# Performance work log

Measured on AMD Instinct MI355X. Metric: run time of the kernel, lower is better.

The kernel has to match this reference:

```python
import jax, jax.numpy as jnp
import numpy as np

N, L, H, E, D = 8, 1024, 16, 1024, 64  # batch, seq_len, heads, embed_size, head_dim


def _xavier(k, shape):
    fan_out, fan_in = shape
    lim = np.sqrt(6.0 / (fan_in + fan_out)).astype(np.float32)
    return jax.random.uniform(k, shape, jnp.float32, -lim, lim)


def setup_inputs() -> dict:
    key = jax.random.key(0)
    ks = jax.random.split(key, 6)
    return {
        "x": jax.random.normal(ks[0], (N, L, E, 1), jnp.float32),
        "Wq": _xavier(ks[1], (D, D)), "bq": jnp.zeros((D,), jnp.float32),
        "Wk": _xavier(ks[2], (D, D)), "bk": jnp.zeros((D,), jnp.float32),
        "Wv": _xavier(ks[3], (D, D)), "bv": jnp.zeros((D,), jnp.float32),
        "Erel": jax.random.normal(ks[4], (1, L, D), jnp.float32),
        "Wo": _xavier(ks[5], (E, E)), "bo": jnp.zeros((E,), jnp.float32),
    }


def _skew(qe):
    # qe: [N, H, L, L] -> pad one zero col on the left, reshape, drop first row
    n, h, l, _ = qe.shape
    p = jnp.pad(qe, ((0, 0), (0, 0), (0, 0), (1, 0)))  # [N,H,L,L+1]
    p = p.reshape(n, h, l + 1, l)
    return p[:, :, 1:, :]  # [N,H,L,L]


def reference(x, Wq, bq, Wk, bk, Wv, bv, Erel, Wo, bo):
    x0 = x[:, :, :, 0]                      # [N, L, E]
    z = x0.reshape(N, L, H, D)              # [N, L, H, D]
    q = z @ Wq.T + bq
    k = z @ Wk.T + bk
    v = z @ Wv.T + bv
    # QE = queries.transpose(1,2) @ E.transpose(1,2): [N,H,L,D] @ [D,L] -> [N,H,L,L]
    QE = jnp.einsum('nlhd,td->nhlt', q, Erel[0])
    # mask_positions: zero where triu(ones,1).flip(1) == 1
    mask = jnp.flip(jnp.triu(jnp.ones((L, L), jnp.float32), 1), axis=1)
    QE = jnp.where(mask == 1, 0.0, QE)
    S = _skew(QE)                           # [N,H,L,L]
    qk = jnp.einsum('nqhd,nkhd->nhqk', q, k)
    attention = jax.nn.softmax(qk / jnp.sqrt(jnp.float32(E)), axis=3) + S
    out = jnp.einsum('nhql,nlhd->nqhd', attention, v).reshape(N, L, H * D)
    return out @ Wo.T + bo                  # [N, L, E]
```

## Files before the change

kernel.cpp:

```cpp
#include <hip/hip_runtime.h>
#include <math.h>

#define N_ 8
#define L_ 1024
#define H_ 16
#define E_ 1024
#define D_ 64

typedef __bf16 bf16x8 __attribute__((ext_vector_type(8)));
typedef __bf16 bf16x4 __attribute__((ext_vector_type(4)));
typedef float  f32x4  __attribute__((ext_vector_type(4)));

#define MFMA16(a, b, c) __builtin_amdgcn_mfma_f32_16x16x32_bf16((a), (b), (c), 0, 0, 0)

#define KSCALE 0.04508422002778011f

__global__ __launch_bounds__(256) void prep_kernel(
    const float* __restrict__ Wo, const float* __restrict__ Erel,
    __bf16* __restrict__ wobf, __bf16* __restrict__ erbf)
{
    const int idx = blockIdx.x * 256 + threadIdx.x;
    const float* src;
    __bf16* dst;
    int off;
    if (blockIdx.x < 1024) { src = Wo;   dst = wobf; off = idx * 4; }
    else                   { src = Erel; dst = erbf; off = (idx - 1024 * 256) * 4; }
    const float4 f = *(const float4*)(src + off);
    bf16x4 h;
    h[0] = (__bf16)f.x; h[1] = (__bf16)f.y; h[2] = (__bf16)f.z; h[3] = (__bf16)f.w;
    *(bf16x4*)(dst + off) = h;
}

__global__ __launch_bounds__(256) void qkv_kernel(
    const float* __restrict__ x,
    const float* __restrict__ Wq, const float* __restrict__ bq,
    const float* __restrict__ Wk, const float* __restrict__ bk,
    const float* __restrict__ Wv, const float* __restrict__ bv,
    __bf16* __restrict__ qo, __bf16* __restrict__ ko, __bf16* __restrict__ vo)
{
    const int t = threadIdx.x, w = t >> 6, lane = t & 63;
    const int quad = lane >> 4, l16 = lane & 15;
    const int m0 = blockIdx.x * 64;

    __shared__ __bf16 xs[64][72];
    __shared__ __bf16 wls[3][64][72];

    #pragma unroll
    for (int i = 0; i < 4; ++i) {
        const int idx = t + i * 256, row = idx >> 4, c4 = idx & 15;
        {
            const float4 f = *(const float4*)(x + (size_t)(m0 + row) * 64 + c4 * 4);
            bf16x4 hh; hh[0]=(__bf16)f.x; hh[1]=(__bf16)f.y; hh[2]=(__bf16)f.z; hh[3]=(__bf16)f.w;
            *(bf16x4*)&xs[row][c4 * 4] = hh;
        }
        {
            const float4 f = *(const float4*)(Wq + (size_t)row * 64 + c4 * 4);
            bf16x4 hh; hh[0]=(__bf16)f.x; hh[1]=(__bf16)f.y; hh[2]=(__bf16)f.z; hh[3]=(__bf16)f.w;
            *(bf16x4*)&wls[0][row][c4 * 4] = hh;
        }
        {
            const float4 f = *(const float4*)(Wk + (size_t)row * 64 + c4 * 4);
            bf16x4 hh; hh[0]=(__bf16)f.x; hh[1]=(__bf16)f.y; hh[2]=(__bf16)f.z; hh[3]=(__bf16)f.w;
            *(bf16x4*)&wls[1][row][c4 * 4] = hh;
        }
        {
            const float4 f = *(const float4*)(Wv + (size_t)row * 64 + c4 * 4);
            bf16x4 hh; hh[0]=(__bf16)f.x; hh[1]=(__bf16)f.y; hh[2]=(__bf16)f.z; hh[3]=(__bf16)f.w;
            *(bf16x4*)&wls[2][row][c4 * 4] = hh;
        }
    }
    __syncthreads();

    bf16x8 a[2];
    a[0] = *(const bf16x8*)&xs[w * 16 + l16][quad * 8];
    a[1] = *(const bf16x8*)&xs[w * 16 + l16][32 + quad * 8];

    f32x4 acc[12];
    const f32x4 zero4 = {0.f, 0.f, 0.f, 0.f};
    #pragma unroll
    for (int nt = 0; nt < 12; ++nt) acc[nt] = zero4;

    #pragma unroll
    for (int nt = 0; nt < 12; ++nt) {
        const int sel = nt >> 2, dt = nt & 3;
        #pragma unroll
        for (int c = 0; c < 2; ++c) {
            const bf16x8 b = *(const bf16x8*)&wls[sel][dt * 16 + l16][c * 32 + quad * 8];
            acc[nt] = MFMA16(a[c], b, acc[nt]);
        }
    }
    __syncthreads();

    __bf16* ts = &wls[0][0][0];
    const float* bias[3] = {bq, bk, bv};
    __bf16* outp[3] = {qo, ko, vo};
    #pragma unroll
    for (int nt = 0; nt < 12; ++nt) {
        const int sel = nt >> 2, dt = nt & 3;
        const float bb = bias[sel][dt * 16 + l16];
        const float scl = (sel == 1) ? KSCALE : 1.0f;
        #pragma unroll
        for (int r = 0; r < 4; ++r)
            ts[(size_t)(w * 16 + quad * 4 + r) * 208 + sel * 64 + dt * 16 + l16] =
                (__bf16)((acc[nt][r] + bb) * scl);
    }
    __syncthreads();
    #pragma unroll
    for (int sel = 0; sel < 3; ++sel)
        #pragma unroll
        for (int i = 0; i < 2; ++i) {
            const int idx = t * 2 + i, row = idx >> 3, c = idx & 7;
            *(float4*)(outp[sel] + (size_t)(m0 + row) * 64 + c * 8) =
                *(const float4*)&ts[(size_t)row * 208 + sel * 64 + c * 8];
        }
}

__global__ __launch_bounds__(256) void vtr_kernel(
    const __bf16* __restrict__ v, __bf16* __restrict__ vt)
{
    const int bid = blockIdx.x;
    const int lt = bid & 15, h = (bid >> 4) & 15, n = bid >> 8;
    const int l0 = lt * 64;
    const int t = threadIdx.x;
    __shared__ __bf16 ls[64][72];

    const int lrow = t & 63, c0 = t >> 6;
    #pragma unroll
    for (int i = 0; i < 2; ++i) {
        const int c = c0 + i * 4;
        union { float4 f; __bf16 hv[8]; } u;
        u.f = *(const float4*)(v + ((size_t)(n * L_ + l0 + lrow) * H_ + h) * D_ + c * 8);
        #pragma unroll
        for (int j = 0; j < 8; ++j) ls[c * 8 + j][lrow] = u.hv[j];
    }
    __syncthreads();
    const int drow0 = t >> 3, lc = t & 7;
    #pragma unroll
    for (int i = 0; i < 2; ++i) {
        const int d = drow0 + i * 32;
        *(float4*)(vt + ((size_t)(n * H_ + h) * D_ + d) * L_ + l0 + lc * 8) =
            *(const float4*)&ls[d][lc * 8];
    }
}

__global__ __launch_bounds__(512, 4) void rel_kernel(
    const __bf16* __restrict__ qbf, const __bf16* __restrict__ vtrb,
    const __bf16* __restrict__ erbf, __bf16* __restrict__ rbuf)
{
    const int bid = blockIdx.x;
    const int qt = 3 - (bid >> 7);
    const int p = bid & 127;
    const int h = p & 15, n = p >> 4;
    const int q0 = qt * 256;
    const int t = threadIdx.x, w = t >> 6, lane = t & 63;
    const int quad = lane >> 4, l16 = lane & 15;

    __shared__ __bf16 vt[2][64][72];
    __shared__ __bf16 rs[128][72];

    const int qA = q0 + w * 16;
    const size_t qoffA = ((size_t)(n * L_ + qA + l16) * H_ + h) * D_;
    const size_t qoffB = qoffA + (size_t)128 * H_ * D_;
    const bf16x8 qaA0 = *(const bf16x8*)(qbf + qoffA + quad * 8);
    const bf16x8 qaA1 = *(const bf16x8*)(qbf + qoffA + 32 + quad * 8);
    const bf16x8 qaB0 = *(const bf16x8*)(qbf + qoffB + quad * 8);
    const bf16x8 qaB1 = *(const bf16x8*)(qbf + qoffB + 32 + quad * 8);

    const __bf16* vbase = vtrb + ((size_t)(n * H_ + h) * D_) * L_;
    const int srow = t >> 3, sc8 = (t & 7) * 8;
    const int ktmax = qt * 4 + 4;

    float4 vreg = *(const float4*)(vbase + (size_t)srow * 1024 + sc8);
    *(float4*)&vt[0][srow][sc8] = vreg;
    vreg = *(const float4*)(vbase + 64 + (size_t)srow * 1024 + sc8);
    __syncthreads();

    const f32x4 zero4 = {0.f, 0.f, 0.f, 0.f};
    f32x4 OrA[4], OrB[4];
    #pragma unroll
    for (int nt = 0; nt < 4; ++nt) { OrA[nt] = zero4; OrB[nt] = zero4; }

    for (int kt = 0; kt < ktmax; ++kt) {
        const int cur = kt & 1;
        if (kt + 1 < ktmax) {
            *(float4*)&vt[cur ^ 1][srow][sc8] = vreg;
            if (kt + 2 < ktmax)
                vreg = *(const float4*)(vbase + (kt + 2) * 64
                                        + (size_t)srow * 1024 + sc8);
        }

        const bool dorelA = (kt * 64 <= qA + 15);
        const bool dorelB = (kt * 64 <= qA + 128 + 15);
        bf16x8 rbA0, rbA1, rbB0, rbB1;

        if (dorelA) {
            const int tb = kt * 64 + 1008 - qA;
            #pragma unroll
            for (int st = 0; st < 5; ++st) {
                int tr = tb + st * 16 + l16;
                tr = tr > 1023 ? 1023 : tr;
                const __bf16* er = erbf + (size_t)tr * 64;
                f32x4 acc = zero4;
                acc = MFMA16(*(const bf16x8*)(er + quad * 8), qaA0, acc);
                acc = MFMA16(*(const bf16x8*)(er + 32 + quad * 8), qaA1, acc);
                #pragma unroll
                for (int r = 0; r < 4; ++r) {
                    const int kc = st * 16 + quad * 4 + r + l16 - 15;
                    const int tg = tb + st * 16 + quad * 4 + r;
                    if (kc >= 0 && kc < 64)
                        rs[w * 16 + l16][kc] = (tg <= 1023) ? (__bf16)acc[r]
                                                            : (__bf16)0.0f;
                }
            }
            rbA0 = *(const bf16x8*)&rs[w * 16 + l16][quad * 8];
            rbA1 = *(const bf16x8*)&rs[w * 16 + l16][32 + quad * 8];
        }
        if (dorelB) {
            const int tb = kt * 64 + 1008 - (qA + 128);
            #pragma unroll
            for (int st = 0; st < 5; ++st) {
                int tr = tb + st * 16 + l16;
                tr = tr > 1023 ? 1023 : tr;
                const __bf16* er = erbf + (size_t)tr * 64;
                f32x4 acc = zero4;
                acc = MFMA16(*(const bf16x8*)(er + quad * 8), qaB0, acc);
                acc = MFMA16(*(const bf16x8*)(er + 32 + quad * 8), qaB1, acc);
                #pragma unroll
                for (int r = 0; r < 4; ++r) {
                    const int kc = st * 16 + quad * 4 + r + l16 - 15;
                    const int tg = tb + st * 16 + quad * 4 + r;
                    if (kc >= 0 && kc < 64)
                        rs[w * 16 + l16][kc] = (tg <= 1023) ? (__bf16)acc[r]
                                                            : (__bf16)0.0f;
                }
            }
            rbB0 = *(const bf16x8*)&rs[w * 16 + l16][quad * 8];
            rbB1 = *(const bf16x8*)&rs[w * 16 + l16][32 + quad * 8];
        }

        #pragma unroll
        for (int nt = 0; nt < 4; ++nt) {
            const bf16x8 va0 = *(const bf16x8*)&vt[cur][nt * 16 + l16][quad * 8];
            const bf16x8 va1 = *(const bf16x8*)&vt[cur][nt * 16 + l16][32 + quad * 8];
            if (dorelA) {
                OrA[nt] = MFMA16(va0, rbA0, OrA[nt]);
                OrA[nt] = MFMA16(va1, rbA1, OrA[nt]);
            }
            if (dorelB) {
                OrB[nt] = MFMA16(va0, rbB0, OrB[nt]);
                OrB[nt] = MFMA16(va1, rbB1, OrB[nt]);
            }
        }
        __syncthreads();
    }

    const int erow = lane >> 3, ec8 = lane & 7;
    #pragma unroll
    for (int nt = 0; nt < 4; ++nt) {
        bf16x4 ov;
        #pragma unroll
        for (int r = 0; r < 4; ++r) ov[r] = (__bf16)OrA[nt][r];
        *(bf16x4*)&rs[w * 16 + l16][nt * 16 + quad * 4] = ov;
    }
    #pragma unroll
    for (int i = 0; i < 2; ++i) {
        const int r = erow + i * 8;
        *(float4*)(rbuf + ((size_t)(n * L_ + qA + r)) * E_ + h * 64 + ec8 * 8) =
            *(const float4*)&rs[w * 16 + r][ec8 * 8];
    }
    #pragma unroll
    for (int nt = 0; nt < 4; ++nt) {
        bf16x4 ov;
        #pragma unroll
        for (int r = 0; r < 4; ++r) ov[r] = (__bf16)OrB[nt][r];
        *(bf16x4*)&rs[w * 16 + l16][nt * 16 + quad * 4] = ov;
    }
    #pragma unroll
    for (int i = 0; i < 2; ++i) {
        const int r = erow + i * 8;
        *(float4*)(rbuf + ((size_t)(n * L_ + qA + 128 + r)) * E_ + h * 64 + ec8 * 8) =
            *(const float4*)&rs[w * 16 + r][ec8 * 8];
    }
}

__global__ __launch_bounds__(512, 4) void flash_kernel(
    const __bf16* __restrict__ qbf, const __bf16* __restrict__ kbf,
    const __bf16* __restrict__ vtrb, const __bf16* __restrict__ rbuf,
    __bf16* __restrict__ attnA)
{
    const int bid = blockIdx.x;
    const int qt = bid >> 7;
    const int p = bid & 127;
    const int h = p & 15, n = p >> 4;
    const int q0 = qt * 256;
    const int t = threadIdx.x, w = t >> 6, lane = t & 63;
    const int quad = lane >> 4, l16 = lane & 15;

    __shared__ __bf16 ks[2][64][72];
    __shared__ __bf16 vt[2][64][72];
    __shared__ __bf16 ps[128][72];

    const int qA = q0 + w * 16;
    const size_t qoffA = ((size_t)(n * L_ + qA + l16) * H_ + h) * D_;
    const size_t qoffB = qoffA + (size_t)128 * H_ * D_;
    const bf16x8 qaA0 = *(const bf16x8*)(qbf + qoffA + quad * 8);
    const bf16x8 qaA1 = *(const bf16x8*)(qbf + qoffA + 32 + quad * 8);
    const bf16x8 qaB0 = *(const bf16x8*)(qbf + qoffB + quad * 8);
    const bf16x8 qaB1 = *(const bf16x8*)(qbf + qoffB + 32 + quad * 8);

    const __bf16* kbase = kbf + ((size_t)n * L_ * H_ + h) * D_;
    const __bf16* vbase = vtrb + ((size_t)(n * H_ + h) * D_) * L_;
    const int srow = t >> 3, sc8 = (t & 7) * 8;

    float4 kreg = *(const float4*)(kbase + (size_t)srow * 1024 + sc8);
    float4 vreg = *(const float4*)(vbase + (size_t)srow * 1024 + sc8);
    *(float4*)&ks[0][srow][sc8] = kreg;
    *(float4*)&vt[0][srow][sc8] = vreg;
    kreg = *(const float4*)(kbase + 64 * 1024 + (size_t)srow * 1024 + sc8);
    vreg = *(const float4*)(vbase + 64 + (size_t)srow * 1024 + sc8);
    __syncthreads();

    const f32x4 zero4 = {0.f, 0.f, 0.f, 0.f};
    f32x4 OsA[4], OsB[4];
    #pragma unroll
    for (int nt = 0; nt < 4; ++nt) { OsA[nt] = zero4; OsB[nt] = zero4; }
    float esumA = 0.f, esumB = 0.f;

    for (int kt = 0; kt < 16; ++kt) {
        const int cur = kt & 1;
        if (kt < 15) {
            *(float4*)&ks[cur ^ 1][srow][sc8] = kreg;
            *(float4*)&vt[cur ^ 1][srow][sc8] = vreg;
            if (kt < 14) {
                kreg = *(const float4*)(kbase + (size_t)(kt + 2) * 64 * 1024
                                        + (size_t)srow * 1024 + sc8);
                vreg = *(const float4*)(vbase + (kt + 2) * 64
                                        + (size_t)srow * 1024 + sc8);
            }
        }

        f32x4 sA[4], sB[4];
        #pragma unroll
        for (int nt = 0; nt < 4; ++nt) {
            const bf16x8 ka0 = *(const bf16x8*)&ks[cur][nt * 16 + l16][quad * 8];
            const bf16x8 ka1 = *(const bf16x8*)&ks[cur][nt * 16 + l16][32 + quad * 8];
            f32x4 a = zero4;
            a = MFMA16(ka0, qaA0, a);
            a = MFMA16(ka1, qaA1, a);
            sA[nt] = a;
            f32x4 b = zero4;
            b = MFMA16(ka0, qaB0, b);
            b = MFMA16(ka1, qaB1, b);
            sB[nt] = b;
        }

        #pragma unroll
        for (int nt = 0; nt < 4; ++nt) {
            bf16x4 pk;
            #pragma unroll
            for (int r = 0; r < 4; ++r) {
                const float e = exp2f(sA[nt][r]);
                esumA += e;
                pk[r] = (__bf16)e;
            }
            *(bf16x4*)&ps[w * 16 + l16][nt * 16 + quad * 4] = pk;
        }
        const bf16x8 pbA0 = *(const bf16x8*)&ps[w * 16 + l16][quad * 8];
        const bf16x8 pbA1 = *(const bf16x8*)&ps[w * 16 + l16][32 + quad * 8];
        #pragma unroll
        for (int nt = 0; nt < 4; ++nt) {
            bf16x4 pk;
            #pragma unroll
            for (int r = 0; r < 4; ++r) {
                const float e = exp2f(sB[nt][r]);
                esumB += e;
                pk[r] = (__bf16)e;
            }
            *(bf16x4*)&ps[w * 16 + l16][nt * 16 + quad * 4] = pk;
        }
        const bf16x8 pbB0 = *(const bf16x8*)&ps[w * 16 + l16][quad * 8];
        const bf16x8 pbB1 = *(const bf16x8*)&ps[w * 16 + l16][32 + quad * 8];

        #pragma unroll
        for (int nt = 0; nt < 4; ++nt) {
            const bf16x8 va0 = *(const bf16x8*)&vt[cur][nt * 16 + l16][quad * 8];
            const bf16x8 va1 = *(const bf16x8*)&vt[cur][nt * 16 + l16][32 + quad * 8];
            OsA[nt] = MFMA16(va0, pbA0, OsA[nt]);
            OsA[nt] = MFMA16(va1, pbA1, OsA[nt]);
            OsB[nt] = MFMA16(va0, pbB0, OsB[nt]);
            OsB[nt] = MFMA16(va1, pbB1, OsB[nt]);
        }
        __syncthreads();
    }

    esumA += __shfl_xor(esumA, 16, 64);
    esumA += __shfl_xor(esumA, 32, 64);
    esumB += __shfl_xor(esumB, 16, 64);
    esumB += __shfl_xor(esumB, 32, 64);
    const float invlA = 1.0f / esumA;
    const float invlB = 1.0f / esumB;
    const int erow = lane >> 3, ec8 = lane & 7;

    #pragma unroll
    for (int nt = 0; nt < 4; ++nt) {
        bf16x4 ov;
        #pragma unroll
        for (int r = 0; r < 4; ++r) ov[r] = (__bf16)(OsA[nt][r] * invlA);
        *(bf16x4*)&ps[w * 16 + l16][nt * 16 + quad * 4] = ov;
    }
    #pragma unroll
    for (int i = 0; i < 2; ++i) {
        const int r = erow + i * 8;
        const size_t goff = ((size_t)(n * L_ + qA + r)) * E_ + h * 64 + ec8 * 8;
        union { float4 f; __bf16 hv[8]; } ua, ub, uo;
        ua.f = *(const float4*)&ps[w * 16 + r][ec8 * 8];
        ub.f = *(const float4*)(rbuf + goff);
        #pragma unroll
        for (int j = 0; j < 8; ++j)
            uo.hv[j] = (__bf16)((float)ua.hv[j] + (float)ub.hv[j]);
        *(float4*)(attnA + goff) = uo.f;
    }
    #pragma unroll
    for (int nt = 0; nt < 4; ++nt) {
        bf16x4 ov;
        #pragma unroll
        for (int r = 0; r < 4; ++r) ov[r] = (__bf16)(OsB[nt][r] * invlB);
        *(bf16x4*)&ps[w * 16 + l16][nt * 16 + quad * 4] = ov;
    }
    #pragma unroll
    for (int i = 0; i < 2; ++i) {
        const int r = erow + i * 8;
        const size_t goff = ((size_t)(n * L_ + qA + 128 + r)) * E_ + h * 64 + ec8 * 8;
        union { float4 f; __bf16 hv[8]; } ua, ub, uo;
        ua.f = *(const float4*)&ps[w * 16 + r][ec8 * 8];
        ub.f = *(const float4*)(rbuf + goff);
        #pragma unroll
        for (int j = 0; j < 8; ++j)
            uo.hv[j] = (__bf16)((float)ua.hv[j] + (float)ub.hv[j]);
        *(float4*)(attnA + goff) = uo.f;
    }
}

__global__ __launch_bounds__(256) void proj_kernel(
    const __bf16* __restrict__ A, const __bf16* __restrict__ W,
    const float* __restrict__ bo, float* __restrict__ out)
{
    const int bid = blockIdx.x;
    const int rt = bid >> 3, ct = bid & 7;
    const int r0 = rt * 128, c0 = ct * 128;
    const int t = threadIdx.x, w = t >> 6, lane = t & 63;
    const int quad = lane >> 4, l16 = lane & 15;
    const int wm = w >> 1, wn = w & 1;

    __shared__ __bf16 As[128 * 64];
    __shared__ __bf16 Bs[128 * 64];

    f32x4 acc[16];
    const f32x4 zero4 = {0.f, 0.f, 0.f, 0.f};
    #pragma unroll
    for (int i = 0; i < 16; ++i) acc[i] = zero4;

    const int lrow = lane >> 3, lcg = lane & 7;

    for (int kt = 0; kt < 16; ++kt) {
        const int e0 = kt * 64;
        __syncthreads();
        #pragma unroll
        for (int i = 0; i < 4; ++i) {
            const int chunk = w * 4 + i;
            const int row = chunk * 8 + lrow;
            const __bf16* ga = A + (size_t)(r0 + row) * E_ + e0 + lcg * 8;
            const __bf16* gb = W + (size_t)(c0 + row) * E_ + e0 + lcg * 8;
            __builtin_amdgcn_global_load_lds(
                (const __attribute__((address_space(1))) void*)ga,
                (__attribute__((address_space(3))) void*)&As[chunk * 512], 16, 0, 0);
            __builtin_amdgcn_global_load_lds(
                (const __attribute__((address_space(1))) void*)gb,
                (__attribute__((address_space(3))) void*)&Bs[chunk * 512], 16, 0, 0);
        }
        __syncthreads();
        #pragma unroll
        for (int c = 0; c < 2; ++c) {
            bf16x8 am[4], bn[4];
            #pragma unroll
            for (int i = 0; i < 4; ++i) {
                am[i] = *(const bf16x8*)&As[(wm * 64 + i * 16 + l16) * 64 + c * 32 + quad * 8];
                bn[i] = *(const bf16x8*)&Bs[(wn * 64 + i * 16 + l16) * 64 + c * 32 + quad * 8];
            }
            #pragma unroll
            for (int i = 0; i < 4; ++i)
                #pragma unroll
                for (int j = 0; j < 4; ++j)
                    acc[i * 4 + j] = MFMA16(am[i], bn[j], acc[i * 4 + j]);
        }
    }

    #pragma unroll
    for (int i = 0; i < 4; ++i)
        #pragma unroll
        for (int j = 0; j < 4; ++j) {
            const int col = c0 + wn * 64 + j * 16 + l16;
            const float bb = bo[col];
            #pragma unroll
            for (int r = 0; r < 4; ++r)
                out[(size_t)(r0 + wm * 64 + i * 16 + quad * 4 + r) * E_ + col] =
                    acc[i * 4 + j][r] + bb;
        }
}

extern "C" void kernel_launch(void* const* d_in, const int* in_sizes, int n_in,
                              void* d_out, int out_size, void* d_ws, size_t ws_size,
                              hipStream_t stream)
{
    const float* x    = (const float*)d_in[0];
    const float* Wq   = (const float*)d_in[1];
    const float* bq   = (const float*)d_in[2];
    const float* Wk   = (const float*)d_in[3];
    const float* bk   = (const float*)d_in[4];
    const float* Wv   = (const float*)d_in[5];
    const float* bv   = (const float*)d_in[6];
    const float* Erel = (const float*)d_in[7];
    const float* Wo   = (const float*)d_in[8];
    const float* bo   = (const float*)d_in[9];
    float* out = (float*)d_out;

    char* p = (char*)d_ws;
    __bf16* qbf   = (__bf16*)p; p += (size_t)N_ * L_ * H_ * D_ * 2;
    __bf16* kbf   = (__bf16*)p; p += (size_t)N_ * L_ * H_ * D_ * 2;
    __bf16* vbf   = (__bf16*)p; p += (size_t)N_ * L_ * H_ * D_ * 2;
    __bf16* vtrb  = (__bf16*)p; p += (size_t)N_ * L_ * H_ * D_ * 2;
    __bf16* attnA = (__bf16*)p; p += (size_t)N_ * L_ * E_ * 2;
    __bf16* rbuf  = (__bf16*)p; p += (size_t)N_ * L_ * E_ * 2;
    __bf16* wobf  = (__bf16*)p; p += (size_t)E_ * E_ * 2;
    __bf16* erbf  = (__bf16*)p; p += (size_t)L_ * D_ * 2;

    prep_kernel<<<1088, 256, 0, stream>>>(Wo, Erel, wobf, erbf);
    qkv_kernel<<<(N_ * L_ * H_) / 64, 256, 0, stream>>>(x, Wq, bq, Wk, bk, Wv, bv,
                                                        qbf, kbf, vbf);
    vtr_kernel<<<N_ * H_ * (L_ / 64), 256, 0, stream>>>(vbf, vtrb);
    rel_kernel<<<512, 512, 0, stream>>>(qbf, vtrb, erbf, rbuf);
    flash_kernel<<<512, 512, 0, stream>>>(qbf, kbf, vtrb, rbuf, attnA);
    proj_kernel<<<(N_ * L_ / 128) * (E_ / 128), 256, 0, stream>>>(attnA, wobf, bo, out);
}
```

Measured before the change: 300.4 us.

## Fuse relative-position kernel into flash attention kernel, drop rbuf round trip

Merges rel_kernel into flash_kernel so the skewed QE·V term is accumulated in registers alongside the softmax·V term within the same K/V tile loop. This removes the bf16 rbuf intermediate (write and re-read of N·L·E) and one kernel launch, and reuses the V tiles already in shared memory. Erel is padded with zero rows so the clamping and masking branches go away, and the skew scatter writes into a widened ps buffer at an offset. In exchange the fused kernel uses more registers and shared memory, which may reduce occupancy, and the block ordering changes relative to the old causal-work scheduling.

```diff
diff --git a/kernel.cpp b/kernel.cpp
--- a/kernel.cpp
+++ b/kernel.cpp
@@ -15,16 +15,25 @@
 
 #define KSCALE 0.04508422002778011f
 
+#define ER_ROWS 1104
+
 __global__ __launch_bounds__(256) void prep_kernel(
     const float* __restrict__ Wo, const float* __restrict__ Erel,
     __bf16* __restrict__ wobf, __bf16* __restrict__ erbf)
 {
-    const int idx = blockIdx.x * 256 + threadIdx.x;
+    const int b = blockIdx.x;
+    const int idx = b * 256 + threadIdx.x;
+    if (b >= 1088) {
+        const int off = (idx - 1088 * 256) * 4;
+        bf16x4 z; z[0] = z[1] = z[2] = z[3] = (__bf16)0.0f;
+        *(bf16x4*)(erbf + 1024 * 64 + off) = z;
+        return;
+    }
     const float* src;
     __bf16* dst;
     int off;
-    if (blockIdx.x < 1024) { src = Wo;   dst = wobf; off = idx * 4; }
-    else                   { src = Erel; dst = erbf; off = (idx - 1024 * 256) * 4; }
+    if (b < 1024) { src = Wo;   dst = wobf; off = idx * 4; }
+    else          { src = Erel; dst = erbf; off = (idx - 1024 * 256) * 4; }
     const float4 f = *(const float4*)(src + off);
     bf16x4 h;
     h[0] = (__bf16)f.x; h[1] = (__bf16)f.y; h[2] = (__bf16)f.z; h[3] = (__bf16)f.w;
@@ -143,9 +152,10 @@
     }
 }
 
-__global__ __launch_bounds__(512, 4) void rel_kernel(
-    const __bf16* __restrict__ qbf, const __bf16* __restrict__ vtrb,
-    const __bf16* __restrict__ erbf, __bf16* __restrict__ rbuf)
+__global__ __launch_bounds__(512, 4) void fused_kernel(
+    const __bf16* __restrict__ qbf, const __bf16* __restrict__ kbf,
+    const __bf16* __restrict__ vtrb, const __bf16* __restrict__ erbf,
+    __bf16* __restrict__ attnA)
 {
     const int bid = blockIdx.x;
     const int qt = 3 - (bid >> 7);
@@ -155,8 +165,9 @@
     const int t = threadIdx.x, w = t >> 6, lane = t & 63;
     const int quad = lane >> 4, l16 = lane & 15;
 
+    __shared__ __bf16 ks[2][64][72];
     __shared__ __bf16 vt[2][64][72];
-    __shared__ __bf16 rs[128][72];
+    __shared__ __bf16 ps[128][104];
 
     const int qA = q0 + w * 16;
     const size_t qoffA = ((size_t)(n * L_ + qA + l16) * H_ + h) * D_;
@@ -166,148 +177,6 @@
     const bf16x8 qaB0 = *(const bf16x8*)(qbf + qoffB + quad * 8);
     const bf16x8 qaB1 = *(const bf16x8*)(qbf + qoffB + 32 + quad * 8);
 
-    const __bf16* vbase = vtrb + ((size_t)(n * H_ + h) * D_) * L_;
-    const int srow = t >> 3, sc8 = (t & 7) * 8;
-    const int ktmax = qt * 4 + 4;
-
-    float4 vreg = *(const float4*)(vbase + (size_t)srow * 1024 + sc8);
-    *(float4*)&vt[0][srow][sc8] = vreg;
-    vreg = *(const float4*)(vbase + 64 + (size_t)srow * 1024 + sc8);
-    __syncthreads();
-
-    const f32x4 zero4 = {0.f, 0.f, 0.f, 0.f};
-    f32x4 OrA[4], OrB[4];
-    #pragma unroll
-    for (int nt = 0; nt < 4; ++nt) { OrA[nt] = zero4; OrB[nt] = zero4; }
-
-    for (int kt = 0; kt < ktmax; ++kt) {
-        const int cur = kt & 1;
-        if (kt + 1 < ktmax) {
-            *(float4*)&vt[cur ^ 1][srow][sc8] = vreg;
-            if (kt + 2 < ktmax)
-                vreg = *(const float4*)(vbase + (kt + 2) * 64
-                                        + (size_t)srow * 1024 + sc8);
-        }
-
-        const bool dorelA = (kt * 64 <= qA + 15);
-        const bool dorelB = (kt * 64 <= qA + 128 + 15);
-        bf16x8 rbA0, rbA1, rbB0, rbB1;
-
-        if (dorelA) {
-            const int tb = kt * 64 + 1008 - qA;
-            #pragma unroll
-            for (int st = 0; st < 5; ++st) {
-                int tr = tb + st * 16 + l16;
-                tr = tr > 1023 ? 1023 : tr;
-                const __bf16* er = erbf + (size_t)tr * 64;
-                f32x4 acc = zero4;
-                acc = MFMA16(*(const bf16x8*)(er + quad * 8), qaA0, acc);
-                acc = MFMA16(*(const bf16x8*)(er + 32 + quad * 8), qaA1, acc);
-                #pragma unroll
-                for (int r = 0; r < 4; ++r) {
-                    const int kc = st * 16 + quad * 4 + r + l16 - 15;
-                    const int tg = tb + st * 16 + quad * 4 + r;
-                    if (kc >= 0 && kc < 64)
-                        rs[w * 16 + l16][kc] = (tg <= 1023) ? (__bf16)acc[r]
-                                                            : (__bf16)0.0f;
-                }
-            }
-            rbA0 = *(const bf16x8*)&rs[w * 16 + l16][quad * 8];
-            rbA1 = *(const bf16x8*)&rs[w * 16 + l16][32 + quad * 8];
-        }
-        if (dorelB) {
-            const int tb = kt * 64 + 1008 - (qA + 128);
-            #pragma unroll
-            for (int st = 0; st < 5; ++st) {
-                int tr = tb + st * 16 + l16;
-                tr = tr > 1023 ? 1023 : tr;
-                const __bf16* er = erbf + (size_t)tr * 64;
-                f32x4 acc = zero4;
-                acc = MFMA16(*(const bf16x8*)(er + quad * 8), qaB0, acc);
-                acc = MFMA16(*(const bf16x8*)(er + 32 + quad * 8), qaB1, acc);
-                #pragma unroll
-                for (int r = 0; r < 4; ++r) {
-                    const int kc = st * 16 + quad * 4 + r + l16 - 15;
-                    const int tg = tb + st * 16 + quad * 4 + r;
-                    if (kc >= 0 && kc < 64)
-                        rs[w * 16 + l16][kc] = (tg <= 1023) ? (__bf16)acc[r]
-                                                            : (__bf16)0.0f;
-                }
-            }
-            rbB0 = *(const bf16x8*)&rs[w * 16 + l16][quad * 8];
-            rbB1 = *(const bf16x8*)&rs[w * 16 + l16][32 + quad * 8];
-        }
-
-        #pragma unroll
-        for (int nt = 0; nt < 4; ++nt) {
-            const bf16x8 va0 = *(const bf16x8*)&vt[cur][nt * 16 + l16][quad * 8];
-            const bf16x8 va1 = *(const bf16x8*)&vt[cur][nt * 16 + l16][32 + quad * 8];
-            if (dorelA) {
-                OrA[nt] = MFMA16(va0, rbA0, OrA[nt]);
-                OrA[nt] = MFMA16(va1, rbA1, OrA[nt]);
-            }
-            if (dorelB) {
-                OrB[nt] = MFMA16(va0, rbB0, OrB[nt]);
-                OrB[nt] = MFMA16(va1, rbB1, OrB[nt]);
-            }
-        }
-        __syncthreads();
-    }
-
-    const int erow = lane >> 3, ec8 = lane & 7;
-    #pragma unroll
-    for (int nt = 0; nt < 4; ++nt) {
-        bf16x4 ov;
-        #pragma unroll
-        for (int r = 0; r < 4; ++r) ov[r] = (__bf16)OrA[nt][r];
-        *(bf16x4*)&rs[w * 16 + l16][nt * 16 + quad * 4] = ov;
-    }
-    #pragma unroll
-    for (int i = 0; i < 2; ++i) {
-        const int r = erow + i * 8;
-        *(float4*)(rbuf + ((size_t)(n * L_ + qA + r)) * E_ + h * 64 + ec8 * 8) =
-            *(const float4*)&rs[w * 16 + r][ec8 * 8];
-    }
-    #pragma unroll
-    for (int nt = 0; nt < 4; ++nt) {
-        bf16x4 ov;
-        #pragma unroll
-        for (int r = 0; r < 4; ++r) ov[r] = (__bf16)OrB[nt][r];
-        *(bf16x4*)&rs[w * 16 + l16][nt * 16 + quad * 4] = ov;
-    }
-    #pragma unroll
-    for (int i = 0; i < 2; ++i) {
-        const int r = erow + i * 8;
-        *(float4*)(rbuf + ((size_t)(n * L_ + qA + 128 + r)) * E_ + h * 64 + ec8 * 8) =
-            *(const float4*)&rs[w * 16 + r][ec8 * 8];
-    }
-}
-
-__global__ __launch_bounds__(512, 4) void flash_kernel(
-    const __bf16* __restrict__ qbf, const __bf16* __restrict__ kbf,
-    const __bf16* __restrict__ vtrb, const __bf16* __restrict__ rbuf,
-    __bf16* __restrict__ attnA)
-{
-    const int bid = blockIdx.x;
-    const int qt = bid >> 7;
-    const int p = bid & 127;
-    const int h = p & 15, n = p >> 4;
-    const int q0 = qt * 256;
-    const int t = threadIdx.x, w = t >> 6, lane = t & 63;
-    const int quad = lane >> 4, l16 = lane & 15;
-
-    __shared__ __bf16 ks[2][64][72];
-    __shared__ __bf16 vt[2][64][72];
-    __shared__ __bf16 ps[128][72];
-
-    const int qA = q0 + w * 16;
-    const size_t qoffA = ((size_t)(n * L_ + qA + l16) * H_ + h) * D_;
-    const size_t qoffB = qoffA + (size_t)128 * H_ * D_;
-    const bf16x8 qaA0 = *(const bf16x8*)(qbf + qoffA + quad * 8);
-    const bf16x8 qaA1 = *(const bf16x8*)(qbf + qoffA + 32 + quad * 8);
-    const bf16x8 qaB0 = *(const bf16x8*)(qbf + qoffB + quad * 8);
-    const bf16x8 qaB1 = *(const bf16x8*)(qbf + qoffB + 32 + quad * 8);
-
     const __bf16* kbase = kbf + ((size_t)n * L_ * H_ + h) * D_;
     const __bf16* vbase = vtrb + ((size_t)(n * H_ + h) * D_) * L_;
     const int srow = t >> 3, sc8 = (t & 7) * 8;
@@ -321,9 +190,11 @@
     __syncthreads();
 
     const f32x4 zero4 = {0.f, 0.f, 0.f, 0.f};
-    f32x4 OsA[4], OsB[4];
-    #pragma unroll
-    for (int nt = 0; nt < 4; ++nt) { OsA[nt] = zero4; OsB[nt] = zero4; }
+    f32x4 OsA[4], OsB[4], OrA[4], OrB[4];
+    #pragma unroll
+    for (int nt = 0; nt < 4; ++nt) {
+        OsA[nt] = zero4; OsB[nt] = zero4; OrA[nt] = zero4; OrB[nt] = zero4;
+    }
     float esumA = 0.f, esumB = 0.f;
 
     for (int kt = 0; kt < 16; ++kt) {
@@ -339,7 +210,7 @@
             }
         }
 
-        f32x4 sA[4], sB[4];
+        bf16x4 pkb[4];
         #pragma unroll
         for (int nt = 0; nt < 4; ++nt) {
             const bf16x8 ka0 = *(const bf16x8*)&ks[cur][nt * 16 + l16][quad * 8];
@@ -347,37 +218,29 @@
             f32x4 a = zero4;
             a = MFMA16(ka0, qaA0, a);
             a = MFMA16(ka1, qaA1, a);
-            sA[nt] = a;
             f32x4 b = zero4;
             b = MFMA16(ka0, qaB0, b);
             b = MFMA16(ka1, qaB1, b);
-            sB[nt] = b;
-        }
-
-        #pragma unroll
-        for (int nt = 0; nt < 4; ++nt) {
-            bf16x4 pk;
+            bf16x4 pka;
             #pragma unroll
             for (int r = 0; r < 4; ++r) {
-                const float e = exp2f(sA[nt][r]);
+                const float e = exp2f(a[r]);
                 esumA += e;
-                pk[r] = (__bf16)e;
-            }
-            *(bf16x4*)&ps[w * 16 + l16][nt * 16 + quad * 4] = pk;
+                pka[r] = (__bf16)e;
+            }
+            *(bf16x4*)&ps[w * 16 + l16][nt * 16 + quad * 4] = pka;
+            #pragma unroll
+            for (int r = 0; r < 4; ++r) {
+                const float e = exp2f(b[r]);
+                esumB += e;
+                pkb[nt][r] = (__bf16)e;
+            }
         }
         const bf16x8 pbA0 = *(const bf16x8*)&ps[w * 16 + l16][quad * 8];
         const bf16x8 pbA1 = *(const bf16x8*)&ps[w * 16 + l16][32 + quad * 8];
         #pragma unroll
-        for (int nt = 0; nt < 4; ++nt) {
-            bf16x4 pk;
-            #pragma unroll
-            for (int r = 0; r < 4; ++r) {
-                const float e = exp2f(sB[nt][r]);
-                esumB += e;
-                pk[r] = (__bf16)e;
-            }
-            *(bf16x4*)&ps[w * 16 + l16][nt * 16 + quad * 4] = pk;
-        }
+        for (int nt = 0; nt < 4; ++nt)
+            *(bf16x4*)&ps[w * 16 + l16][nt * 16 + quad * 4] = pkb[nt];
         const bf16x8 pbB0 = *(const bf16x8*)&ps[w * 16 + l16][quad * 8];
         const bf16x8 pbB1 = *(const bf16x8*)&ps[w * 16 + l16][32 + quad * 8];
 
@@ -390,6 +253,60 @@
             OsB[nt] = MFMA16(va0, pbB0, OsB[nt]);
             OsB[nt] = MFMA16(va1, pbB1, OsB[nt]);
         }
+
+        const bool dorelA = (kt * 64 <= qA + 15);
+        const bool dorelB = (kt * 64 <= qA + 143);
+        bf16x8 rbA0 = {}, rbA1 = {}, rbB0 = {}, rbB1 = {};
+        if (dorelA) {
+            const int tb = kt * 64 + 1008 - qA;
+            #pragma unroll
+            for (int st = 0; st < 5; ++st) {
+                const __bf16* er = erbf + (size_t)(tb + st * 16 + l16) * 64;
+                f32x4 acc = zero4;
+                acc = MFMA16(*(const bf16x8*)(er + quad * 8), qaA0, acc);
+                acc = MFMA16(*(const bf16x8*)(er + 32 + quad * 8), qaA1, acc);
+                #pragma unroll
+                for (int r = 0; r < 4; ++r)
+                    ps[w * 16 + l16][st * 16 + quad * 4 + r + l16 + 1] = (__bf16)acc[r];
+            }
+            rbA0 = *(const bf16x8*)&ps[w * 16 + l16][16 + quad * 8];
+            rbA1 = *(const bf16x8*)&ps[w * 16 + l16][48 + quad * 8];
+        }
+        if (dorelB) {
+            const int tb = kt * 64 + 880 - qA;
+            #pragma unroll
+            for (int st = 0; st < 5; ++st) {
+                const __bf16* er = erbf + (size_t)(tb + st * 16 + l16) * 64;
+                f32x4 acc = zero4;
+                acc = MFMA16(*(const bf16x8*)(er + quad * 8), qaB0, acc);
+                acc = MFMA16(*(const bf16x8*)(er + 32 + quad * 8), qaB1, acc);
+                #pragma unroll
+                for (int r = 0; r < 4; ++r)
+                    ps[w * 16 + l16][st * 16 + quad * 4 + r + l16 + 1] = (__bf16)acc[r];
+            }
+            rbB0 = *(const bf16x8*)&ps[w * 16 + l16][16 + quad * 8];
+            rbB1 = *(const bf16x8*)&ps[w * 16 + l16][48 + quad * 8];
+        }
+
+        if (dorelA) {
+            #pragma unroll
+            for (int nt = 0; nt < 4; ++nt) {
+                const bf16x8 va0 = *(const bf16x8*)&vt[cur][nt * 16 + l16][quad * 8];
+                const bf16x8 va1 = *(const bf16x8*)&vt[cur][nt * 16 + l16][32 + quad * 8];
+                OrA[nt] = MFMA16(va0, rbA0, OrA[nt]);
+                OrA[nt] = MFMA16(va1, rbA1, OrA[nt]);
+                OrB[nt] = MFMA16(va0, rbB0, OrB[nt]);
+                OrB[nt] = MFMA16(va1, rbB1, OrB[nt]);
+            }
+        } else if (dorelB) {
+            #pragma unroll
+            for (int nt = 0; nt < 4; ++nt) {
+                const bf16x8 va0 = *(const bf16x8*)&vt[cur][nt * 16 + l16][quad * 8];
+                const bf16x8 va1 = *(const bf16x8*)&vt[cur][nt * 16 + l16][32 + quad * 8];
+                OrB[nt] = MFMA16(va0, rbB0, OrB[nt]);
+                OrB[nt] = MFMA16(va1, rbB1, OrB[nt]);
+            }
+        }
         __syncthreads();
     }
 
@@ -405,39 +322,29 @@
     for (int nt = 0; nt < 4; ++nt) {
         bf16x4 ov;
         #pragma unroll
-        for (int r = 0; r < 4; ++r) ov[r] = (__bf16)(OsA[nt][r] * invlA);
+        for (int r = 0; r < 4; ++r)
+            ov[r] = (__bf16)(OsA[nt][r] * invlA + OrA[nt][r]);
         *(bf16x4*)&ps[w * 16 + l16][nt * 16 + quad * 4] = ov;
     }
     #pragma unroll
     for (int i = 0; i < 2; ++i) {
         const int r = erow + i * 8;
-        const size_t goff = ((size_t)(n * L_ + qA + r)) * E_ + h * 64 + ec8 * 8;
-        union { float4 f; __bf16 hv[8]; } ua, ub, uo;
-        ua.f = *(const float4*)&ps[w * 16 + r][ec8 * 8];
-        ub.f = *(const float4*)(rbuf + goff);
-        #pragma unroll
-        for (int j = 0; j < 8; ++j)
-            uo.hv[j] = (__bf16)((float)ua.hv[j] + (float)ub.hv[j]);
-        *(float4*)(attnA + goff) = uo.f;
+        *(float4*)(attnA + ((size_t)(n * L_ + qA + r)) * E_ + h * 64 + ec8 * 8) =
+            *(const float4*)&ps[w * 16 + r][ec8 * 8];
     }
     #pragma unroll
     for (int nt = 0; nt < 4; ++nt) {
         bf16x4 ov;
         #pragma unroll
-        for (int r = 0; r < 4; ++r) ov[r] = (__bf16)(OsB[nt][r] * invlB);
+        for (int r = 0; r < 4; ++r)
+            ov[r] = (__bf16)(OsB[nt][r] * invlB + OrB[nt][r]);
         *(bf16x4*)&ps[w * 16 + l16][nt * 16 + quad * 4] = ov;
     }
     #pragma unroll
     for (int i = 0; i < 2; ++i) {
         const int r = erow + i * 8;
-        const size_t goff = ((size_t)(n * L_ + qA + 128 + r)) * E_ + h * 64 + ec8 * 8;
-        union { float4 f; __bf16 hv[8]; } ua, ub, uo;
-        ua.f = *(const float4*)&ps[w * 16 + r][ec8 * 8];
-        ub.f = *(const float4*)(rbuf + goff);
-        #pragma unroll
-        for (int j = 0; j < 8; ++j)
-            uo.hv[j] = (__bf16)((float)ua.hv[j] + (float)ub.hv[j]);
-        *(float4*)(attnA + goff) = uo.f;
+        *(float4*)(attnA + ((size_t)(n * L_ + qA + 128 + r)) * E_ + h * 64 + ec8 * 8) =
+            *(const float4*)&ps[w * 16 + r][ec8 * 8];
     }
 }
 
@@ -530,15 +437,13 @@
     __bf16* vbf   = (__bf16*)p; p += (size_t)N_ * L_ * H_ * D_ * 2;
     __bf16* vtrb  = (__bf16*)p; p += (size_t)N_ * L_ * H_ * D_ * 2;
     __bf16* attnA = (__bf16*)p; p += (size_t)N_ * L_ * E_ * 2;
-    __bf16* rbuf  = (__bf16*)p; p += (size_t)N_ * L_ * E_ * 2;
     __bf16* wobf  = (__bf16*)p; p += (size_t)E_ * E_ * 2;
-    __bf16* erbf  = (__bf16*)p; p += (size_t)L_ * D_ * 2;
-
-    prep_kernel<<<1088, 256, 0, stream>>>(Wo, Erel, wobf, erbf);
+    __bf16* erbf  = (__bf16*)p; p += (size_t)ER_ROWS * D_ * 2;
+
+    prep_kernel<<<1093, 256, 0, stream>>>(Wo, Erel, wobf, erbf);
     qkv_kernel<<<(N_ * L_ * H_) / 64, 256, 0, stream>>>(x, Wq, bq, Wk, bk, Wv, bv,
                                                         qbf, kbf, vbf);
     vtr_kernel<<<N_ * H_ * (L_ / 64), 256, 0, stream>>>(vbf, vtrb);
-    rel_kernel<<<512, 512, 0, stream>>>(qbf, vtrb, erbf, rbuf);
-    flash_kernel<<<512, 512, 0, stream>>>(qbf, kbf, vtrb, rbuf, attnA);
+    fused_kernel<<<512, 512, 0, stream>>>(qbf, kbf, vtrb, erbf, attnA);
     proj_kernel<<<(N_ * L_ / 128) * (E_ / 128), 256, 0, stream>>>(attnA, wobf, bo, out);
 }
```

Result: slower. 388.5 us (+29.3%).
